# Kernel tuning notes

Hardware: AMD Instinct MI355X
Metric: run time of the kernel (lower is better)

Reference implementation:

```python
import jax, jax.numpy as jnp
import numpy as np

EPS = 1e-12  # torch F.normalize eps

def _l2norm(t, axis):
    n = jnp.linalg.norm(t, axis=axis, keepdims=True)
    return t / jnp.maximum(n, EPS)

def setup_inputs() -> dict:
    key = jax.random.key(0)
    ks = jax.random.split(key, 7)
    B, L, D, F, K = 16, 128, 512, 1024, 16
    return {
        "x": jax.random.normal(ks[0], (B, L, D), jnp.float32),
        "W_gate_basis": jax.random.normal(ks[1], (K, D, F), jnp.float32) * (1.0 / np.sqrt(D)),
        "W_up_basis": jax.random.normal(ks[2], (K, D, F), jnp.float32) * (1.0 / np.sqrt(D)),
        "W_down_basis": jax.random.normal(ks[3], (K, F, D), jnp.float32) * (1.0 / np.sqrt(F)),
        "token_coef1": jax.random.normal(ks[4], (L, K), jnp.float32),
        "token_coef2": jax.random.normal(ks[5], (L, K), jnp.float32),
        "token_coef3": jax.random.normal(ks[6], (L, K), jnp.float32),
        "u_scale_param": jnp.ones((1, F), jnp.float32),
        "v_scale_param": jnp.ones((1, F), jnp.float32),
    }

def reference(x, W_gate_basis, W_up_basis, W_down_basis,
              token_coef1, token_coef2, token_coef3,
              u_scale_param, v_scale_param):
    D = x.shape[-1]
    c1 = jax.nn.softmax(token_coef1, axis=-1)
    c2 = jax.nn.softmax(token_coef2, axis=-1)
    c3 = jax.nn.softmax(token_coef3, axis=-1)
    # per-token weights [L, D, F] / [L, F, D]
    W_gate = jnp.einsum('lk,kio->lio', c1, W_gate_basis)
    W_up = jnp.einsum('lk,kio->lio', c2, W_up_basis)
    W_down = jnp.einsum('lk,koj->loj', c3, W_down_basis)
    W_gate = _l2norm(W_gate, axis=1)   # normalize over input dim D
    W_up = _l2norm(W_up, axis=1)
    W_down = _l2norm(W_down, axis=1)   # normalize over hidden dim F
    u = jnp.einsum('bld,ldf->blf', x, W_gate)
    v = jnp.einsum('bld,ldf->blf', x, W_up)
    u_scale = jnp.abs(u_scale_param) * 1.0
    v_scale = jnp.abs(v_scale_param) * jnp.sqrt(jnp.float32(D))
    h = jax.nn.silu(v_scale * v) * (u_scale * u)
    out = jnp.einsum('blf,lfd->bld', h, W_down)
    return _l2norm(out, axis=-1)
```

## Files before the change

kernel.cpp:

```cpp
#include <hip/hip_runtime.h>
#include <hip/hip_bf16.h>
#include <cmath>


typedef _Float16 half8 __attribute__((ext_vector_type(8)));
typedef _Float16 half4 __attribute__((ext_vector_type(4)));
typedef float    f32x4 __attribute__((ext_vector_type(4)));

#define MFMA_F16 __builtin_amdgcn_mfma_f32_16x16x32_f16

static constexpr size_t OFF_P1 = 0;
static constexpr size_t OFF_P2 = 16777216;
static constexpr size_t OFF_P3 = 33554432;
static constexpr size_t OFF_HP = 50331648;
static constexpr size_t WS_FAST = OFF_HP + 4194304;

__global__ __launch_bounds__(256) void prep_basis_all(
    const float* __restrict__ wg, const float* __restrict__ wu,
    const float* __restrict__ wd,
    _Float16* __restrict__ P1, _Float16* __restrict__ P2,
    _Float16* __restrict__ P3, int zoff)
{
    int z = blockIdx.y + zoff;
    const float* src = (z == 0) ? wg : (z == 1) ? wu : wd;
    _Float16*    dst = (z == 0) ? P1 : (z == 1) ? P2 : P3;
    int Amin = (z == 2) ? 1024 : 512;
    int Bmaj = (z == 2) ? 512 : 1024;
    int nM = Bmaj >> 4;
    int m0 = (blockIdx.x / nM) * 32;
    int M0 = (blockIdx.x % nM) * 16;

    __shared__ float S[16 * 544];
    int t = threadIdx.x;

    int row = (t >> 2) & 31;
    int cg  = t & 3;
    int khi = t >> 7;
#pragma unroll
    for (int p = 0; p < 8; ++p) {
        int k = p * 2 + khi;
        f32x4 v = *(const f32x4*)(
            src + (size_t)k * Amin * Bmaj + (size_t)(m0 + row) * Bmaj + M0 + cg * 4);
#pragma unroll
        for (int j = 0; j < 4; ++j)
            S[k * 544 + row * 17 + cg * 4 + j] = v[j];
    }
    __syncthreads();

    int mn = t & 31, mjb = t >> 5;
#pragma unroll
    for (int q = 0; q < 2; ++q) {
        int mj = mjb + q * 8;
        half8 v0, v1;
#pragma unroll
        for (int k = 0; k < 8; ++k) v0[k] = (_Float16)S[k * 544 + mn * 17 + mj];
#pragma unroll
        for (int k = 0; k < 8; ++k) v1[k] = (_Float16)S[(k + 8) * 544 + mn * 17 + mj];
        _Float16* out = dst + ((size_t)(M0 + mj) * Amin + m0 + mn) * 16;
        *(half8*)out       = v0;
        *(half8*)(out + 8) = v1;
    }
}

__global__ __launch_bounds__(256) void prep_x(
    const float* __restrict__ x, _Float16* __restrict__ XA)
{
    int idx = blockIdx.x * 256 + threadIdx.x;
    int d4 = idx & 127;
    int l  = (idx >> 7) & 127;
    int b  = idx >> 14;
    f32x4 v = *(const f32x4*)(x + ((size_t)(b * 128 + l) * 512 + d4 * 4));
    half4 h = { (_Float16)v[0], (_Float16)v[1], (_Float16)v[2], (_Float16)v[3] };
    *(half4*)(XA + ((size_t)(l * 16 + b) * 512 + d4 * 4)) = h;
}

__global__ __launch_bounds__(256, 2) void up_fast(
    const _Float16* __restrict__ P1, const _Float16* __restrict__ P2,
    const _Float16* __restrict__ XA,
    const float* __restrict__ tc1, const float* __restrict__ tc2,
    const float* __restrict__ usp, const float* __restrict__ vsp,
    _Float16* __restrict__ Hp)
{
    int lg = blockIdx.x >> 6;
    int f0 = (blockIdx.x & 63) * 16;
    int tid = threadIdx.x;
    int w = tid >> 6, lane = tid & 63;
    int n = lane & 15, kc = lane >> 4;

    __shared__ __align__(16) _Float16 Wt[2][16 * 584];
    __shared__ float CN[2 * 256];

    if (tid < 32) {
        int s = tid >> 4, ll = tid & 15;
        const float* row = (s ? tc2 : tc1) + (size_t)(lg * 16 + ll) * 16;
        float e[16], m = -1e30f, sum = 0.f;
#pragma unroll
        for (int k = 0; k < 16; ++k) m = fmaxf(m, row[k]);
#pragma unroll
        for (int k = 0; k < 16; ++k) { e[k] = __expf(row[k] - m); sum += e[k]; }
        float r = 1.f / sum;
#pragma unroll
        for (int k = 0; k < 16; ++k) CN[s * 256 + ll * 16 + k] = e[k] * r;
    }
    __syncthreads();

    half8 cf1 = { 0, 0, 0, 0, 0, 0, 0, 0 };
    half8 cf2 = { 0, 0, 0, 0, 0, 0, 0, 0 };
    if (kc < 2) {
#pragma unroll
        for (int j = 0; j < 8; ++j) {
            cf1[j] = (_Float16)CN[0 * 256 + n * 16 + kc * 8 + j];
            cf2[j] = (_Float16)CN[1 * 256 + n * 16 + kc * 8 + j];
        }
    }

    f32x4 zf = { 0.f, 0.f, 0.f, 0.f };
    f32x4 aU[4], aV[4];
#pragma unroll
    for (int i = 0; i < 4; ++i) { aU[i] = zf; aV[i] = zf; }
    float nsqU[4] = { 0.f, 0.f, 0.f, 0.f };
    float nsqV[4] = { 0.f, 0.f, 0.f, 0.f };
    half8 xf[4];
    half8 pa[2][4][2];

    for (int it = 0; it < 16; ++it) {
        int d0 = it * 32;
#pragma unroll
        for (int m = 0; m < 2; ++m) {
            const _Float16* P = m ? P2 : P1;
#pragma unroll
            for (int fl = 0; fl < 4; ++fl)
#pragma unroll
                for (int dg = 0; dg < 2; ++dg) {
                    half8 a = { 0, 0, 0, 0, 0, 0, 0, 0 };
                    if (kc < 2)
                        a = *(const half8*)(P +
                            ((size_t)(f0 + w * 4 + fl) * 512 + d0 + dg * 16 + n) * 16 + kc * 8);
                    pa[m][fl][dg] = a;
                }
        }
        if (it > 0) {
#pragma unroll
            for (int li = 0; li < 4; ++li) {
                int l = w * 4 + li;
                half8 wU = *(const half8*)(&Wt[0][l * 584 + n * 36 + kc * 8]);
                half8 wV = *(const half8*)(&Wt[1][l * 584 + n * 36 + kc * 8]);
                aU[li] = MFMA_F16(xf[li], wU, aU[li], 0, 0, 0);
                aV[li] = MFMA_F16(xf[li], wV, aV[li], 0, 0, 0);
            }
        }
#pragma unroll
        for (int li = 0; li < 4; ++li) {
            int l = lg * 16 + w * 4 + li;
            xf[li] = *(const half8*)(XA + ((size_t)l * 16 + n) * 512 + d0 + kc * 8);
        }
        __syncthreads();
#pragma unroll
        for (int fl = 0; fl < 4; ++fl) {
            int f_l = w * 4 + fl;
#pragma unroll
            for (int dg = 0; dg < 2; ++dg) {
                f32x4 c1 = MFMA_F16(pa[0][fl][dg], cf1, zf, 0, 0, 0);
                nsqU[fl] += c1[0] * c1[0] + c1[1] * c1[1]
                          + c1[2] * c1[2] + c1[3] * c1[3];
                half4 h1 = { (_Float16)c1[0], (_Float16)c1[1],
                             (_Float16)c1[2], (_Float16)c1[3] };
                *(half4*)(&Wt[0][n * 584 + f_l * 36 + dg * 16 + kc * 4]) = h1;
                f32x4 c2 = MFMA_F16(pa[1][fl][dg], cf2, zf, 0, 0, 0);
                nsqV[fl] += c2[0] * c2[0] + c2[1] * c2[1]
                          + c2[2] * c2[2] + c2[3] * c2[3];
                half4 h2 = { (_Float16)c2[0], (_Float16)c2[1],
                             (_Float16)c2[2], (_Float16)c2[3] };
                *(half4*)(&Wt[1][n * 584 + f_l * 36 + dg * 16 + kc * 4]) = h2;
            }
        }
        __syncthreads();
    }
#pragma unroll
    for (int li = 0; li < 4; ++li) {
        int l = w * 4 + li;
        half8 wU = *(const half8*)(&Wt[0][l * 584 + n * 36 + kc * 8]);
        half8 wV = *(const half8*)(&Wt[1][l * 584 + n * 36 + kc * 8]);
        aU[li] = MFMA_F16(xf[li], wU, aU[li], 0, 0, 0);
        aV[li] = MFMA_F16(xf[li], wV, aV[li], 0, 0, 0);
    }

#pragma unroll
    for (int fl = 0; fl < 4; ++fl) {
        float vU = nsqU[fl], vV = nsqV[fl];
        vU += __shfl_xor(vU, 16); vU += __shfl_xor(vU, 32);
        vV += __shfl_xor(vV, 16); vV += __shfl_xor(vV, 32);
        if (kc == 0) {
            CN[0 * 256 + n * 16 + w * 4 + fl] = vU;
            CN[1 * 256 + n * 16 + w * 4 + fl] = vV;
        }
    }
    __syncthreads();

    int f = f0 + n;
    float usv = fabsf(usp[f]);
    float vsv = fabsf(vsp[f]) * 22.627416997969522f;
#pragma unroll
    for (int li = 0; li < 4; ++li) {
        int lgl = lg * 16 + w * 4 + li;
        float r1 = 1.f / fmaxf(sqrtf(CN[0 * 256 + (w * 4 + li) * 16 + n]), 1e-12f);
        float r2 = 1.f / fmaxf(sqrtf(CN[1 * 256 + (w * 4 + li) * 16 + n]), 1e-12f);
#pragma unroll
        for (int i = 0; i < 4; ++i) {
            float u = aU[li][i] * r1;
            float v = aV[li][i] * r2;
            float zz = vsv * v;
            float sil = zz / (1.f + __expf(-zz));
            float h = sil * (usv * u);
            Hp[((size_t)lgl * 16 + kc * 4 + i) * 1024 + f] = (_Float16)h;
        }
    }
}

__global__ __launch_bounds__(256, 2) void down_fast(
    const _Float16* __restrict__ P3, const float* __restrict__ tc3,
    const _Float16* __restrict__ Hp,
    float* __restrict__ Rp, float* __restrict__ Np)
{
    int zh = blockIdx.x >> 8;
    int rem = blockIdx.x & 255;
    int lg = rem >> 5;
    int d0 = (rem & 31) * 16;
    int tid = threadIdx.x;
    int w = tid >> 6, lane = tid & 63;
    int n = lane & 15, kc = lane >> 4;

    __shared__ __align__(16) _Float16 Wt[16 * 584];
    __shared__ float CN[256];

    if (tid < 16) {
        const float* row = tc3 + (size_t)(lg * 16 + tid) * 16;
        float e[16], m = -1e30f, sum = 0.f;
#pragma unroll
        for (int k = 0; k < 16; ++k) m = fmaxf(m, row[k]);
#pragma unroll
        for (int k = 0; k < 16; ++k) { e[k] = __expf(row[k] - m); sum += e[k]; }
        float r = 1.f / sum;
#pragma unroll
        for (int k = 0; k < 16; ++k) CN[tid * 16 + k] = e[k] * r;
    }
    __syncthreads();

    half8 cf3 = { 0, 0, 0, 0, 0, 0, 0, 0 };
    if (kc < 2) {
#pragma unroll
        for (int j = 0; j < 8; ++j)
            cf3[j] = (_Float16)CN[n * 16 + kc * 8 + j];
    }

    f32x4 zf = { 0.f, 0.f, 0.f, 0.f };
    f32x4 aO[4];
#pragma unroll
    for (int i = 0; i < 4; ++i) aO[i] = zf;
    float nsqD[4] = { 0.f, 0.f, 0.f, 0.f };
    half8 hf[4];
    half8 pa[4][2];

    for (int it = 0; it < 8; ++it) {
        int f0 = zh * 256 + it * 32;
#pragma unroll
        for (int dl = 0; dl < 4; ++dl) {
#pragma unroll
            for (int fg = 0; fg < 2; ++fg) {
                half8 a = { 0, 0, 0, 0, 0, 0, 0, 0 };
                if (kc < 2)
                    a = *(const half8*)(P3 +
                        ((size_t)(d0 + w * 4 + dl) * 1024 + f0 + fg * 16 + n) * 16 + kc * 8);
                pa[dl][fg] = a;
            }
        }
        if (it > 0) {
#pragma unroll
            for (int li = 0; li < 4; ++li) {
                int l = w * 4 + li;
                half8 wf = *(const half8*)(&Wt[l * 584 + n * 36 + kc * 8]);
                aO[li] = MFMA_F16(hf[li], wf, aO[li], 0, 0, 0);
            }
        }
#pragma unroll
        for (int li = 0; li < 4; ++li) {
            int l = lg * 16 + w * 4 + li;
            hf[li] = *(const half8*)(Hp + ((size_t)l * 16 + n) * 1024 + f0 + kc * 8);
        }
        __syncthreads();
#pragma unroll
        for (int dl = 0; dl < 4; ++dl) {
            int d_l = w * 4 + dl;
#pragma unroll
            for (int fg = 0; fg < 2; ++fg) {
                f32x4 cw = MFMA_F16(pa[dl][fg], cf3, zf, 0, 0, 0);
                nsqD[dl] += cw[0] * cw[0] + cw[1] * cw[1]
                          + cw[2] * cw[2] + cw[3] * cw[3];
                half4 h4 = { (_Float16)cw[0], (_Float16)cw[1],
                             (_Float16)cw[2], (_Float16)cw[3] };
                *(half4*)(&Wt[n * 584 + d_l * 36 + fg * 16 + kc * 4]) = h4;
            }
        }
        __syncthreads();
    }
#pragma unroll
    for (int li = 0; li < 4; ++li) {
        int l = w * 4 + li;
        half8 wf = *(const half8*)(&Wt[l * 584 + n * 36 + kc * 8]);
        aO[li] = MFMA_F16(hf[li], wf, aO[li], 0, 0, 0);
    }

#pragma unroll
    for (int dl = 0; dl < 4; ++dl) {
        float v = nsqD[dl];
        v += __shfl_xor(v, 16); v += __shfl_xor(v, 32);
        if (kc == 0)
            Np[(size_t)zh * 65536 + (size_t)(lg * 16 + n) * 512 + d0 + w * 4 + dl] = v;
    }
#pragma unroll
    for (int li = 0; li < 4; ++li) {
        int lgl = lg * 16 + w * 4 + li;
#pragma unroll
        for (int i = 0; i < 4; ++i)
            Rp[(size_t)zh * 1048576 +
               ((size_t)(kc * 4 + i) * 128 + lgl) * 512 + d0 + n] = aO[li][i];
    }
}

__global__ __launch_bounds__(128) void final_combine(
    const float* __restrict__ Rp, const float* __restrict__ Np,
    float* __restrict__ out)
{
    int rid = blockIdx.x;
    int l = rid & 127;
    int t = threadIdx.x;
    f32x4 r = { 0.f, 0.f, 0.f, 0.f };
    f32x4 nn = { 0.f, 0.f, 0.f, 0.f };
#pragma unroll
    for (int zh = 0; zh < 4; ++zh) {
        f32x4 rz = *(const f32x4*)(Rp + (size_t)zh * 1048576 + (size_t)rid * 512 + t * 4);
        f32x4 nz = *(const f32x4*)(Np + (size_t)zh * 65536 + (size_t)l * 512 + t * 4);
#pragma unroll
        for (int j = 0; j < 4; ++j) { r[j] += rz[j]; nn[j] += nz[j]; }
    }
    f32x4 y;
#pragma unroll
    for (int j = 0; j < 4; ++j) {
        float rr = 1.f / fmaxf(sqrtf(fmaxf(nn[j], 0.f)), 1e-12f);
        y[j] = r[j] * rr;
    }
    float s = y[0] * y[0] + y[1] * y[1] + y[2] * y[2] + y[3] * y[3];
#pragma unroll
    for (int off = 32; off > 0; off >>= 1) s += __shfl_down(s, off);
    __shared__ float sred[2];
    if ((t & 63) == 0) sred[t >> 6] = s;
    __syncthreads();
    float rr = 1.f / fmaxf(sqrtf(sred[0] + sred[1]), 1e-12f);
    f32x4 o = { y[0] * rr, y[1] * rr, y[2] * rr, y[3] * rr };
    *(f32x4*)(out + (size_t)rid * 512 + t * 4) = o;
}

__global__ __launch_bounds__(256) void up_kernel(
    const float* __restrict__ x,
    const float* __restrict__ wg, const float* __restrict__ wu,
    const float* __restrict__ tc1, const float* __restrict__ tc2,
    const float* __restrict__ usp, const float* __restrict__ vsp,
    _Float16* __restrict__ Hp)
{
    int lg = blockIdx.x >> 6;
    int f0 = (blockIdx.x & 63) * 16;
    int tid = threadIdx.x;
    int w = tid >> 6, lane = tid & 63;
    int n = lane & 15, kc = lane >> 4;

    __shared__ __align__(16) _Float16 Xt[256 * 40];
    __shared__ __align__(16) _Float16 Bh[32 * 16 * 24];
    __shared__ __align__(16) _Float16 Wt[16 * 528];
    __shared__ float CN[2 * 16 * 16];

    if (tid < 32) {
        int s = tid >> 4, ll = tid & 15;
        const float* row = (s ? tc2 : tc1) + (size_t)(lg * 16 + ll) * 16;
        float e[16], m = -1e30f, sum = 0.f;
#pragma unroll
        for (int k = 0; k < 16; ++k) m = fmaxf(m, row[k]);
#pragma unroll
        for (int k = 0; k < 16; ++k) { e[k] = __expf(row[k] - m); sum += e[k]; }
        float r = 1.f / sum;
#pragma unroll
        for (int k = 0; k < 16; ++k) CN[s * 256 + ll * 16 + k] = e[k] * r;
    }
    __syncthreads();

    half8 cf1 = { 0, 0, 0, 0, 0, 0, 0, 0 };
    half8 cf2 = { 0, 0, 0, 0, 0, 0, 0, 0 };
    if (kc < 2) {
#pragma unroll
        for (int j = 0; j < 8; ++j) {
            cf1[j] = (_Float16)CN[0 * 256 + n * 16 + kc * 8 + j];
            cf2[j] = (_Float16)CN[1 * 256 + n * 16 + kc * 8 + j];
        }
    }

    f32x4 zf = { 0.f, 0.f, 0.f, 0.f };
    f32x4 aU[4], aV[4];
#pragma unroll
    for (int i = 0; i < 4; ++i) { aU[i] = zf; aV[i] = zf; }
    float nsqU[4] = { 0.f, 0.f, 0.f, 0.f };
    float nsqV[4] = { 0.f, 0.f, 0.f, 0.f };

    for (int it = 0; it < 16; ++it) {
        int d0 = it * 32;
#pragma unroll
        for (int p = 0; p < 8; ++p) {
            int r = p * 32 + (tid >> 3);
            int fj = tid & 7;
            int ll = r >> 4, b = r & 15;
            f32x4 v = *(const f32x4*)(
                x + ((size_t)(b * 128 + lg * 16 + ll) * 512 + d0 + fj * 4));
            half4 h = { (_Float16)v[0], (_Float16)v[1],
                        (_Float16)v[2], (_Float16)v[3] };
            *(half4*)(&Xt[r * 40 + fj * 4]) = h;
        }
#pragma unroll
        for (int p = 0; p < 8; ++p) {
            int idx = p * 256 + tid;
            int q = idx & 3, dd = (idx >> 2) & 31, k = idx >> 7;
            f32x4 v = *(const f32x4*)(
                wg + ((size_t)k * 512 + d0 + dd) * 1024 + f0 + q * 4);
#pragma unroll
            for (int j = 0; j < 4; ++j)
                Bh[(dd * 16 + q * 4 + j) * 24 + k] = (_Float16)v[j];
        }
        __syncthreads();
#pragma unroll
        for (int fl = 0; fl < 4; ++fl) {
            int f_l = w * 4 + fl;
#pragma unroll
            for (int dg = 0; dg < 2; ++dg) {
                half8 a = { 0, 0, 0, 0, 0, 0, 0, 0 };
                if (kc < 2)
                    a = *(const half8*)(&Bh[((dg * 16 + n) * 16 + f_l) * 24 + kc * 8]);
                f32x4 cw = MFMA_F16(a, cf1, zf, 0, 0, 0);
                nsqU[fl] += cw[0] * cw[0] + cw[1] * cw[1]
                          + cw[2] * cw[2] + cw[3] * cw[3];
                half4 h4 = { (_Float16)cw[0], (_Float16)cw[1],
                             (_Float16)cw[2], (_Float16)cw[3] };
                *(half4*)(&Wt[n * 528 + f_l * 32 + dg * 16 + kc * 4]) = h4;
            }
        }
        __syncthreads();
#pragma unroll
        for (int li = 0; li < 4; ++li) {
            int l = w * 4 + li;
            half8 xf = *(const half8*)(&Xt[(l * 16 + n) * 40 + kc * 8]);
            half8 wf = *(const half8*)(&Wt[l * 528 + n * 32 + kc * 8]);
            aU[li] = MFMA_F16(xf, wf, aU[li], 0, 0, 0);
        }
#pragma unroll
        for (int p = 0; p < 8; ++p) {
            int idx = p * 256 + tid;
            int q = idx & 3, dd = (idx >> 2) & 31, k = idx >> 7;
            f32x4 v = *(const f32x4*)(
                wu + ((size_t)k * 512 + d0 + dd) * 1024 + f0 + q * 4);
#pragma unroll
            for (int j = 0; j < 4; ++j)
                Bh[(dd * 16 + q * 4 + j) * 24 + k] = (_Float16)v[j];
        }
        __syncthreads();
#pragma unroll
        for (int fl = 0; fl < 4; ++fl) {
            int f_l = w * 4 + fl;
#pragma unroll
            for (int dg = 0; dg < 2; ++dg) {
                half8 a = { 0, 0, 0, 0, 0, 0, 0, 0 };
                if (kc < 2)
                    a = *(const half8*)(&Bh[((dg * 16 + n) * 16 + f_l) * 24 + kc * 8]);
                f32x4 cw = MFMA_F16(a, cf2, zf, 0, 0, 0);
                nsqV[fl] += cw[0] * cw[0] + cw[1] * cw[1]
                          + cw[2] * cw[2] + cw[3] * cw[3];
                half4 h4 = { (_Float16)cw[0], (_Float16)cw[1],
                             (_Float16)cw[2], (_Float16)cw[3] };
                *(half4*)(&Wt[n * 528 + f_l * 32 + dg * 16 + kc * 4]) = h4;
            }
        }
        __syncthreads();
#pragma unroll
        for (int li = 0; li < 4; ++li) {
            int l = w * 4 + li;
            half8 xf = *(const half8*)(&Xt[(l * 16 + n) * 40 + kc * 8]);
            half8 wf = *(const half8*)(&Wt[l * 528 + n * 32 + kc * 8]);
            aV[li] = MFMA_F16(xf, wf, aV[li], 0, 0, 0);
        }
        __syncthreads();
    }

#pragma unroll
    for (int fl = 0; fl < 4; ++fl) {
        float vU = nsqU[fl], vV = nsqV[fl];
        vU += __shfl_xor(vU, 16); vU += __shfl_xor(vU, 32);
        vV += __shfl_xor(vV, 16); vV += __shfl_xor(vV, 32);
        if (kc == 0) {
            CN[0 * 256 + n * 16 + w * 4 + fl] = vU;
            CN[1 * 256 + n * 16 + w * 4 + fl] = vV;
        }
    }
    __syncthreads();

    int f = f0 + n;
    float usv = fabsf(usp[f]);
    float vsv = fabsf(vsp[f]) * 22.627416997969522f;
#pragma unroll
    for (int li = 0; li < 4; ++li) {
        int lgl = lg * 16 + w * 4 + li;
        float r1 = 1.f / fmaxf(sqrtf(CN[0 * 256 + (w * 4 + li) * 16 + n]), 1e-12f);
        float r2 = 1.f / fmaxf(sqrtf(CN[1 * 256 + (w * 4 + li) * 16 + n]), 1e-12f);
#pragma unroll
        for (int i = 0; i < 4; ++i) {
            float u = aU[li][i] * r1;
            float v = aV[li][i] * r2;
            float zz = vsv * v;
            float sil = zz / (1.f + __expf(-zz));
            float h = sil * (usv * u);
            Hp[((size_t)lgl * 16 + kc * 4 + i) * 1024 + f] = (_Float16)h;
        }
    }
}

__global__ __launch_bounds__(256) void down_kernel(
    const float* __restrict__ wd, const float* __restrict__ tc3,
    const _Float16* __restrict__ Hp, float* __restrict__ out)
{
    int lg = blockIdx.x >> 5;
    int d0 = (blockIdx.x & 31) * 16;
    int tid = threadIdx.x;
    int w = tid >> 6, lane = tid & 63;
    int n = lane & 15, kc = lane >> 4;

    __shared__ __align__(16) _Float16 Ht[256 * 40];
    __shared__ __align__(16) _Float16 Bh[32 * 16 * 24];
    __shared__ __align__(16) _Float16 Wt[16 * 528];
    __shared__ float CN[16 * 16];

    if (tid < 16) {
        const float* row = tc3 + (size_t)(lg * 16 + tid) * 16;
        float e[16], m = -1e30f, sum = 0.f;
#pragma unroll
        for (int k = 0; k < 16; ++k) m = fmaxf(m, row[k]);
#pragma unroll
        for (int k = 0; k < 16; ++k) { e[k] = __expf(row[k] - m); sum += e[k]; }
        float r = 1.f / sum;
#pragma unroll
        for (int k = 0; k < 16; ++k) CN[tid * 16 + k] = e[k] * r;
    }
    __syncthreads();

    half8 cf3 = { 0, 0, 0, 0, 0, 0, 0, 0 };
    if (kc < 2) {
#pragma unroll
        for (int j = 0; j < 8; ++j)
            cf3[j] = (_Float16)CN[n * 16 + kc * 8 + j];
    }

    f32x4 zf = { 0.f, 0.f, 0.f, 0.f };
    f32x4 aO[4];
#pragma unroll
    for (int i = 0; i < 4; ++i) aO[i] = zf;
    float nsqD[4] = { 0.f, 0.f, 0.f, 0.f };

    for (int it = 0; it < 32; ++it) {
        int f0 = it * 32;
#pragma unroll
        for (int p = 0; p < 8; ++p) {
            int r = p * 32 + (tid >> 3);
            int hj = tid & 7;
            int ll = r >> 4, b = r & 15;
            half4 v = *(const half4*)(
                Hp + ((size_t)(lg * 16 + ll) * 16 + b) * 1024 + f0 + hj * 4);
            *(half4*)(&Ht[r * 40 + hj * 4]) = v;
        }
#pragma unroll
        for (int p = 0; p < 8; ++p) {
            int idx = p * 256 + tid;
            int q = idx & 3, ff = (idx >> 2) & 31, k = idx >> 7;
            f32x4 v = *(const f32x4*)(
                wd + ((size_t)k * 1024 + f0 + ff) * 512 + d0 + q * 4);
#pragma unroll
            for (int j = 0; j < 4; ++j)
                Bh[(ff * 16 + q * 4 + j) * 24 + k] = (_Float16)v[j];
        }
        __syncthreads();
#pragma unroll
        for (int dl = 0; dl < 4; ++dl) {
            int d_l = w * 4 + dl;
#pragma unroll
            for (int fg = 0; fg < 2; ++fg) {
                half8 a = { 0, 0, 0, 0, 0, 0, 0, 0 };
                if (kc < 2)
                    a = *(const half8*)(&Bh[((fg * 16 + n) * 16 + d_l) * 24 + kc * 8]);
                f32x4 cw = MFMA_F16(a, cf3, zf, 0, 0, 0);
                nsqD[dl] += cw[0] * cw[0] + cw[1] * cw[1]
                          + cw[2] * cw[2] + cw[3] * cw[3];
                half4 h4 = { (_Float16)cw[0], (_Float16)cw[1],
                             (_Float16)cw[2], (_Float16)cw[3] };
                *(half4*)(&Wt[n * 528 + d_l * 32 + fg * 16 + kc * 4]) = h4;
            }
        }
        __syncthreads();
#pragma unroll
        for (int li = 0; li < 4; ++li) {
            int l = w * 4 + li;
            half8 hf = *(const half8*)(&Ht[(l * 16 + n) * 40 + kc * 8]);
            half8 wf = *(const half8*)(&Wt[l * 528 + n * 32 + kc * 8]);
            aO[li] = MFMA_F16(hf, wf, aO[li], 0, 0, 0);
        }
        __syncthreads();
    }

#pragma unroll
    for (int dl = 0; dl < 4; ++dl) {
        float v = nsqD[dl];
        v += __shfl_xor(v, 16); v += __shfl_xor(v, 32);
        if (kc == 0) CN[n * 16 + w * 4 + dl] = v;
    }
    __syncthreads();

#pragma unroll
    for (int li = 0; li < 4; ++li) {
        int lgl = lg * 16 + w * 4 + li;
        float r3 = 1.f / fmaxf(sqrtf(CN[(w * 4 + li) * 16 + n]), 1e-12f);
#pragma unroll
        for (int i = 0; i < 4; ++i)
            out[((size_t)(kc * 4 + i) * 128 + lgl) * 512 + d0 + n] = aO[li][i] * r3;
    }
}

__global__ __launch_bounds__(128) void final_kernel(float* __restrict__ out)
{
    int rid = blockIdx.x;
    int t = threadIdx.x;
    f32x4 y = *(const f32x4*)(out + (size_t)rid * 512 + t * 4);
    float s = y[0] * y[0] + y[1] * y[1] + y[2] * y[2] + y[3] * y[3];
#pragma unroll
    for (int off = 32; off > 0; off >>= 1) s += __shfl_down(s, off);
    __shared__ float sred[2];
    if ((t & 63) == 0) sred[t >> 6] = s;
    __syncthreads();
    float rr = 1.f / fmaxf(sqrtf(sred[0] + sred[1]), 1e-12f);
    f32x4 o = { y[0] * rr, y[1] * rr, y[2] * rr, y[3] * rr };
    *(f32x4*)(out + (size_t)rid * 512 + t * 4) = o;
}

extern "C" void kernel_launch(void* const* d_in, const int* in_sizes, int n_in,
                              void* d_out, int out_size, void* d_ws, size_t ws_size,
                              hipStream_t stream)
{
    (void)in_sizes; (void)n_in; (void)out_size;
    const float* x   = (const float*)d_in[0];
    const float* wg  = (const float*)d_in[1];
    const float* wu  = (const float*)d_in[2];
    const float* wd  = (const float*)d_in[3];
    const float* tc1 = (const float*)d_in[4];
    const float* tc2 = (const float*)d_in[5];
    const float* tc3 = (const float*)d_in[6];
    const float* usp = (const float*)d_in[7];
    const float* vsp = (const float*)d_in[8];
    float* outp = (float*)d_out;
    char* ws = (char*)d_ws;

    if (ws_size >= WS_FAST) {
        _Float16* P1 = (_Float16*)(ws + OFF_P1);
        _Float16* P2 = (_Float16*)(ws + OFF_P2);
        _Float16* P3 = (_Float16*)(ws + OFF_P3);
        _Float16* XA = (_Float16*)(ws + OFF_P3);
        _Float16* Hp = (_Float16*)(ws + OFF_HP);
        float* Rp = (float*)(ws + OFF_P1);
        float* Np = (float*)(ws + OFF_P2);
        prep_basis_all<<<dim3(1024, 2), dim3(256), 0, stream>>>(
            wg, wu, wd, P1, P2, P3, 0);
        prep_x<<<dim3(1024), dim3(256), 0, stream>>>(x, XA);
        up_fast<<<dim3(512), dim3(256), 0, stream>>>(P1, P2, XA, tc1, tc2,
                                                     usp, vsp, Hp);
        prep_basis_all<<<dim3(1024, 1), dim3(256), 0, stream>>>(
            wg, wu, wd, P1, P2, P3, 2);
        down_fast<<<dim3(1024), dim3(256), 0, stream>>>(P3, tc3, Hp, Rp, Np);
        final_combine<<<dim3(2048), dim3(128), 0, stream>>>(Rp, Np, outp);
    } else {
        _Float16* Hp = (_Float16*)ws;
        up_kernel<<<dim3(512), dim3(256), 0, stream>>>(x, wg, wu, tc1, tc2,
                                                       usp, vsp, Hp);
        down_kernel<<<dim3(256), dim3(256), 0, stream>>>(wd, tc3, Hp, outp);
        final_kernel<<<dim3(2048), dim3(128), 0, stream>>>(outp);
    }
}
```

Baseline: 233.9 us.

## Split up_fast reduction dimension across two wavegroups with LDS combine

Doubles the up_fast block to 512 threads. Two groups of four waves each handle half of the D reduction, and group 1's partial accumulators and norm sums go through shared memory to group 0, which applies the normalization and SiLU epilogue. The aim is more waves per CU to hide load and MFMA latency in the 16-iteration serial loop. In exchange, LDS use per block doubles and an extra cross-group reduction with barriers is added, which may limit occupancy.

```diff
diff --git a/kernel.cpp b/kernel.cpp
--- a/kernel.cpp
+++ b/kernel.cpp
@@ -74,7 +74,7 @@
     *(half4*)(XA + ((size_t)(l * 16 + b) * 512 + d4 * 4)) = h;
 }
 
-__global__ __launch_bounds__(256, 2) void up_fast(
+__global__ __launch_bounds__(512, 4) void up_fast(
     const _Float16* __restrict__ P1, const _Float16* __restrict__ P2,
     const _Float16* __restrict__ XA,
     const float* __restrict__ tc1, const float* __restrict__ tc2,
@@ -84,11 +84,13 @@
     int lg = blockIdx.x >> 6;
     int f0 = (blockIdx.x & 63) * 16;
     int tid = threadIdx.x;
-    int w = tid >> 6, lane = tid & 63;
+    int g = tid >> 8;
+    int w = (tid >> 6) & 3;
+    int lane = tid & 63;
     int n = lane & 15, kc = lane >> 4;
 
-    __shared__ __align__(16) _Float16 Wt[2][16 * 584];
-    __shared__ float CN[2 * 256];
+    __shared__ __align__(16) _Float16 Wt[2][2][16 * 584];
+    __shared__ float CN[4 * 256];
 
     if (tid < 32) {
         int s = tid >> 4, ll = tid & 15;
@@ -123,8 +125,8 @@
     half8 xf[4];
     half8 pa[2][4][2];
 
-    for (int it = 0; it < 16; ++it) {
-        int d0 = it * 32;
+    for (int it = 0; it < 8; ++it) {
+        int d0 = (g << 8) + it * 32;
 #pragma unroll
         for (int m = 0; m < 2; ++m) {
             const _Float16* P = m ? P2 : P1;
@@ -143,8 +145,8 @@
 #pragma unroll
             for (int li = 0; li < 4; ++li) {
                 int l = w * 4 + li;
-                half8 wU = *(const half8*)(&Wt[0][l * 584 + n * 36 + kc * 8]);
-                half8 wV = *(const half8*)(&Wt[1][l * 584 + n * 36 + kc * 8]);
+                half8 wU = *(const half8*)(&Wt[g][0][l * 584 + n * 36 + kc * 8]);
+                half8 wV = *(const half8*)(&Wt[g][1][l * 584 + n * 36 + kc * 8]);
                 aU[li] = MFMA_F16(xf[li], wU, aU[li], 0, 0, 0);
                 aV[li] = MFMA_F16(xf[li], wV, aV[li], 0, 0, 0);
             }
@@ -165,13 +167,13 @@
                           + c1[2] * c1[2] + c1[3] * c1[3];
                 half4 h1 = { (_Float16)c1[0], (_Float16)c1[1],
                              (_Float16)c1[2], (_Float16)c1[3] };
-                *(half4*)(&Wt[0][n * 584 + f_l * 36 + dg * 16 + kc * 4]) = h1;
+                *(half4*)(&Wt[g][0][n * 584 + f_l * 36 + dg * 16 + kc * 4]) = h1;
                 f32x4 c2 = MFMA_F16(pa[1][fl][dg], cf2, zf, 0, 0, 0);
                 nsqV[fl] += c2[0] * c2[0] + c2[1] * c2[1]
                           + c2[2] * c2[2] + c2[3] * c2[3];
                 half4 h2 = { (_Float16)c2[0], (_Float16)c2[1],
                              (_Float16)c2[2], (_Float16)c2[3] };
-                *(half4*)(&Wt[1][n * 584 + f_l * 36 + dg * 16 + kc * 4]) = h2;
+                *(half4*)(&Wt[g][1][n * 584 + f_l * 36 + dg * 16 + kc * 4]) = h2;
             }
         }
         __syncthreads();
@@ -179,8 +181,8 @@
 #pragma unroll
     for (int li = 0; li < 4; ++li) {
         int l = w * 4 + li;
-        half8 wU = *(const half8*)(&Wt[0][l * 584 + n * 36 + kc * 8]);
-        half8 wV = *(const half8*)(&Wt[1][l * 584 + n * 36 + kc * 8]);
+        half8 wU = *(const half8*)(&Wt[g][0][l * 584 + n * 36 + kc * 8]);
+        half8 wV = *(const half8*)(&Wt[g][1][l * 584 + n * 36 + kc * 8]);
         aU[li] = MFMA_F16(xf[li], wU, aU[li], 0, 0, 0);
         aV[li] = MFMA_F16(xf[li], wV, aV[li], 0, 0, 0);
     }
@@ -191,28 +193,48 @@
         vU += __shfl_xor(vU, 16); vU += __shfl_xor(vU, 32);
         vV += __shfl_xor(vV, 16); vV += __shfl_xor(vV, 32);
         if (kc == 0) {
-            CN[0 * 256 + n * 16 + w * 4 + fl] = vU;
-            CN[1 * 256 + n * 16 + w * 4 + fl] = vV;
-        }
-    }
-    __syncthreads();
-
-    int f = f0 + n;
-    float usv = fabsf(usp[f]);
-    float vsv = fabsf(vsp[f]) * 22.627416997969522f;
-#pragma unroll
-    for (int li = 0; li < 4; ++li) {
-        int lgl = lg * 16 + w * 4 + li;
-        float r1 = 1.f / fmaxf(sqrtf(CN[0 * 256 + (w * 4 + li) * 16 + n]), 1e-12f);
-        float r2 = 1.f / fmaxf(sqrtf(CN[1 * 256 + (w * 4 + li) * 16 + n]), 1e-12f);
-#pragma unroll
-        for (int i = 0; i < 4; ++i) {
-            float u = aU[li][i] * r1;
-            float v = aV[li][i] * r2;
-            float zz = vsv * v;
-            float sil = zz / (1.f + __expf(-zz));
-            float h = sil * (usv * u);
-            Hp[((size_t)lgl * 16 + kc * 4 + i) * 1024 + f] = (_Float16)h;
+            CN[(g << 9) + 0 * 256 + n * 16 + w * 4 + fl] = vU;
+            CN[(g << 9) + 1 * 256 + n * 16 + w * 4 + fl] = vV;
+        }
+    }
+    __syncthreads();
+
+    float* XB = (float*)(&Wt[1][0][0]);
+    if (g == 1) {
+#pragma unroll
+        for (int li = 0; li < 4; ++li)
+#pragma unroll
+            for (int i = 0; i < 4; ++i) {
+                int idx = ((w * 4 + li) * 16 + kc * 4 + i) * 16 + n;
+                XB[idx]        = aU[li][i];
+                XB[4096 + idx] = aV[li][i];
+            }
+    }
+    __syncthreads();
+
+    if (g == 0) {
+        int f = f0 + n;
+        float usv = fabsf(usp[f]);
+        float vsv = fabsf(vsp[f]) * 22.627416997969522f;
+#pragma unroll
+        for (int li = 0; li < 4; ++li) {
+            int lgl = lg * 16 + w * 4 + li;
+            float s1 = CN[0 * 256 + (w * 4 + li) * 16 + n]
+                     + CN[512 + 0 * 256 + (w * 4 + li) * 16 + n];
+            float s2 = CN[1 * 256 + (w * 4 + li) * 16 + n]
+                     + CN[512 + 1 * 256 + (w * 4 + li) * 16 + n];
+            float r1 = 1.f / fmaxf(sqrtf(s1), 1e-12f);
+            float r2 = 1.f / fmaxf(sqrtf(s2), 1e-12f);
+#pragma unroll
+            for (int i = 0; i < 4; ++i) {
+                int idx = ((w * 4 + li) * 16 + kc * 4 + i) * 16 + n;
+                float u = (aU[li][i] + XB[idx]) * r1;
+                float v = (aV[li][i] + XB[4096 + idx]) * r2;
+                float zz = vsv * v;
+                float sil = zz / (1.f + __expf(-zz));
+                float h = sil * (usv * u);
+                Hp[((size_t)lgl * 16 + kc * 4 + i) * 1024 + f] = (_Float16)h;
+            }
         }
     }
 }
@@ -679,7 +701,7 @@
         prep_basis_all<<<dim3(1024, 2), dim3(256), 0, stream>>>(
             wg, wu, wd, P1, P2, P3, 0);
         prep_x<<<dim3(1024), dim3(256), 0, stream>>>(x, XA);
-        up_fast<<<dim3(512), dim3(256), 0, stream>>>(P1, P2, XA, tc1, tc2,
+        up_fast<<<dim3(512), dim3(512), 0, stream>>>(P1, P2, XA, tc1, tc2,
                                                      usp, vsp, Hp);
         prep_basis_all<<<dim3(1024, 1), dim3(256), 0, stream>>>(
             wg, wu, wd, P1, P2, P3, 2);
```

Result: slower. 366.0 us (+56.4%).

## Double-buffer LDS weight tiles and prefetch basis; retile X and H for coalesced MFMA loads

Applied to the files above, without the earlier changes.

Double-buffers the shared-memory mixed-weight tiles in up_fast and down_fast, so each iteration writes the next tile while reading the previous one. The basis prefetch for the next step is interleaved between the MFMA phases, which lets one barrier per iteration do the work of two. The X and H intermediates are repacked into an 8-element-chunk interleaved layout, so MFMA operand loads become contiguous 16-byte reads. prep_x now transposes through LDS with fewer blocks. The cost is twice the LDS footprint, which may limit occupancy, and higher register pressure from the prefetched fragments.

```diff
diff --git a/kernel.cpp b/kernel.cpp
--- a/kernel.cpp
+++ b/kernel.cpp
@@ -65,13 +65,28 @@
 __global__ __launch_bounds__(256) void prep_x(
     const float* __restrict__ x, _Float16* __restrict__ XA)
 {
-    int idx = blockIdx.x * 256 + threadIdx.x;
-    int d4 = idx & 127;
-    int l  = (idx >> 7) & 127;
-    int b  = idx >> 14;
-    f32x4 v = *(const f32x4*)(x + ((size_t)(b * 128 + l) * 512 + d4 * 4));
-    half4 h = { (_Float16)v[0], (_Float16)v[1], (_Float16)v[2], (_Float16)v[3] };
-    *(half4*)(XA + ((size_t)(l * 16 + b) * 512 + d4 * 4)) = h;
+    int l = blockIdx.x >> 1, bh = blockIdx.x & 1;
+    __shared__ __align__(16) _Float16 XT[8][524];
+    int t = threadIdx.x;
+
+    int bl = t >> 5, q = t & 31;
+    int b = bh * 8 + bl;
+#pragma unroll
+    for (int j = 0; j < 4; ++j) {
+        f32x4 v = *(const f32x4*)(x + ((size_t)(b * 128 + l) * 512 + j * 128 + q * 4));
+#pragma unroll
+        for (int i = 0; i < 4; ++i)
+            XT[bl][j * 128 + q * 4 + i] = (_Float16)v[i];
+    }
+    __syncthreads();
+
+    int c = t >> 2, bi = t & 3;
+#pragma unroll
+    for (int s = 0; s < 2; ++s) {
+        int blw = bi * 2 + s;
+        half8 h = *(const half8*)(&XT[blw][c * 8]);
+        *(half8*)(XA + (((size_t)(l * 64 + c) * 16 + bh * 8 + blw) * 8)) = h;
+    }
 }
 
 __global__ __launch_bounds__(256, 2) void up_fast(
@@ -87,8 +102,24 @@
     int w = tid >> 6, lane = tid & 63;
     int n = lane & 15, kc = lane >> 4;
 
-    __shared__ __align__(16) _Float16 Wt[2][16 * 584];
+    __shared__ __align__(16) _Float16 Wt[2][2][16 * 584];
     __shared__ float CN[2 * 256];
+
+    half8 pa0[4][2], pa1[4][2];
+#pragma unroll
+    for (int fl = 0; fl < 4; ++fl)
+#pragma unroll
+        for (int dg = 0; dg < 2; ++dg) {
+            half8 a = { 0, 0, 0, 0, 0, 0, 0, 0 };
+            half8 b = { 0, 0, 0, 0, 0, 0, 0, 0 };
+            if (kc < 2) {
+                size_t off = ((size_t)(f0 + w * 4 + fl) * 512 + dg * 16 + n) * 16 + kc * 8;
+                a = *(const half8*)(P1 + off);
+                b = *(const half8*)(P2 + off);
+            }
+            pa0[fl][dg] = a;
+            pa1[fl][dg] = b;
+        }
 
     if (tid < 32) {
         int s = tid >> 4, ll = tid & 15;
@@ -121,66 +152,87 @@
     float nsqU[4] = { 0.f, 0.f, 0.f, 0.f };
     float nsqV[4] = { 0.f, 0.f, 0.f, 0.f };
     half8 xf[4];
-    half8 pa[2][4][2];
 
     for (int it = 0; it < 16; ++it) {
         int d0 = it * 32;
-#pragma unroll
-        for (int m = 0; m < 2; ++m) {
-            const _Float16* P = m ? P2 : P1;
-#pragma unroll
-            for (int fl = 0; fl < 4; ++fl)
-#pragma unroll
-                for (int dg = 0; dg < 2; ++dg) {
-                    half8 a = { 0, 0, 0, 0, 0, 0, 0, 0 };
-                    if (kc < 2)
-                        a = *(const half8*)(P +
-                            ((size_t)(f0 + w * 4 + fl) * 512 + d0 + dg * 16 + n) * 16 + kc * 8);
-                    pa[m][fl][dg] = a;
-                }
-        }
-        if (it > 0) {
-#pragma unroll
-            for (int li = 0; li < 4; ++li) {
-                int l = w * 4 + li;
-                half8 wU = *(const half8*)(&Wt[0][l * 584 + n * 36 + kc * 8]);
-                half8 wV = *(const half8*)(&Wt[1][l * 584 + n * 36 + kc * 8]);
-                aU[li] = MFMA_F16(xf[li], wU, aU[li], 0, 0, 0);
-                aV[li] = MFMA_F16(xf[li], wV, aV[li], 0, 0, 0);
-            }
-        }
-#pragma unroll
-        for (int li = 0; li < 4; ++li) {
-            int l = lg * 16 + w * 4 + li;
-            xf[li] = *(const half8*)(XA + ((size_t)l * 16 + n) * 512 + d0 + kc * 8);
-        }
-        __syncthreads();
+        _Float16* WtA = &Wt[it & 1][0][0];
+        _Float16* WtB = &Wt[it & 1][1][0];
+        const _Float16* RdA = &Wt[(it & 1) ^ 1][0][0];
+        const _Float16* RdB = &Wt[(it & 1) ^ 1][1][0];
+
 #pragma unroll
         for (int fl = 0; fl < 4; ++fl) {
             int f_l = w * 4 + fl;
 #pragma unroll
             for (int dg = 0; dg < 2; ++dg) {
-                f32x4 c1 = MFMA_F16(pa[0][fl][dg], cf1, zf, 0, 0, 0);
+                f32x4 c1 = MFMA_F16(pa0[fl][dg], cf1, zf, 0, 0, 0);
                 nsqU[fl] += c1[0] * c1[0] + c1[1] * c1[1]
                           + c1[2] * c1[2] + c1[3] * c1[3];
                 half4 h1 = { (_Float16)c1[0], (_Float16)c1[1],
                              (_Float16)c1[2], (_Float16)c1[3] };
-                *(half4*)(&Wt[0][n * 584 + f_l * 36 + dg * 16 + kc * 4]) = h1;
-                f32x4 c2 = MFMA_F16(pa[1][fl][dg], cf2, zf, 0, 0, 0);
+                *(half4*)(&WtA[n * 584 + f_l * 36 + dg * 16 + kc * 4]) = h1;
+            }
+        }
+        if (it < 15) {
+#pragma unroll
+            for (int fl = 0; fl < 4; ++fl)
+#pragma unroll
+                for (int dg = 0; dg < 2; ++dg) {
+                    half8 a = { 0, 0, 0, 0, 0, 0, 0, 0 };
+                    if (kc < 2)
+                        a = *(const half8*)(P1 +
+                            ((size_t)(f0 + w * 4 + fl) * 512 + d0 + 32 + dg * 16 + n) * 16 + kc * 8);
+                    pa0[fl][dg] = a;
+                }
+        }
+#pragma unroll
+        for (int fl = 0; fl < 4; ++fl) {
+            int f_l = w * 4 + fl;
+#pragma unroll
+            for (int dg = 0; dg < 2; ++dg) {
+                f32x4 c2 = MFMA_F16(pa1[fl][dg], cf2, zf, 0, 0, 0);
                 nsqV[fl] += c2[0] * c2[0] + c2[1] * c2[1]
                           + c2[2] * c2[2] + c2[3] * c2[3];
                 half4 h2 = { (_Float16)c2[0], (_Float16)c2[1],
                              (_Float16)c2[2], (_Float16)c2[3] };
-                *(half4*)(&Wt[1][n * 584 + f_l * 36 + dg * 16 + kc * 4]) = h2;
-            }
+                *(half4*)(&WtB[n * 584 + f_l * 36 + dg * 16 + kc * 4]) = h2;
+            }
+        }
+        if (it < 15) {
+#pragma unroll
+            for (int fl = 0; fl < 4; ++fl)
+#pragma unroll
+                for (int dg = 0; dg < 2; ++dg) {
+                    half8 a = { 0, 0, 0, 0, 0, 0, 0, 0 };
+                    if (kc < 2)
+                        a = *(const half8*)(P2 +
+                            ((size_t)(f0 + w * 4 + fl) * 512 + d0 + 32 + dg * 16 + n) * 16 + kc * 8);
+                    pa1[fl][dg] = a;
+                }
+        }
+        if (it > 0) {
+#pragma unroll
+            for (int li = 0; li < 4; ++li) {
+                int l = w * 4 + li;
+                half8 wU = *(const half8*)(&RdA[l * 584 + n * 36 + kc * 8]);
+                half8 wV = *(const half8*)(&RdB[l * 584 + n * 36 + kc * 8]);
+                aU[li] = MFMA_F16(xf[li], wU, aU[li], 0, 0, 0);
+                aV[li] = MFMA_F16(xf[li], wV, aV[li], 0, 0, 0);
+            }
+        }
+#pragma unroll
+        for (int li = 0; li < 4; ++li) {
+            int l = lg * 16 + w * 4 + li;
+            xf[li] = *(const half8*)(XA +
+                (((size_t)l * 64 + (d0 >> 3) + kc) * 16 + n) * 8);
         }
         __syncthreads();
     }
 #pragma unroll
     for (int li = 0; li < 4; ++li) {
         int l = w * 4 + li;
-        half8 wU = *(const half8*)(&Wt[0][l * 584 + n * 36 + kc * 8]);
-        half8 wV = *(const half8*)(&Wt[1][l * 584 + n * 36 + kc * 8]);
+        half8 wU = *(const half8*)(&Wt[1][0][l * 584 + n * 36 + kc * 8]);
+        half8 wV = *(const half8*)(&Wt[1][1][l * 584 + n * 36 + kc * 8]);
         aU[li] = MFMA_F16(xf[li], wU, aU[li], 0, 0, 0);
         aV[li] = MFMA_F16(xf[li], wV, aV[li], 0, 0, 0);
     }
@@ -212,7 +264,8 @@
             float zz = vsv * v;
             float sil = zz / (1.f + __expf(-zz));
             float h = sil * (usv * u);
-            Hp[((size_t)lgl * 16 + kc * 4 + i) * 1024 + f] = (_Float16)h;
+            Hp[(((size_t)lgl * 128 + (f >> 3)) * 16 + kc * 4 + i) * 8 + (f & 7)] =
+                (_Float16)h;
         }
     }
 }
@@ -230,8 +283,20 @@
     int w = tid >> 6, lane = tid & 63;
     int n = lane & 15, kc = lane >> 4;
 
-    __shared__ __align__(16) _Float16 Wt[16 * 584];
+    __shared__ __align__(16) _Float16 Wt[2][16 * 584];
     __shared__ float CN[256];
+
+    half8 pa[4][2];
+#pragma unroll
+    for (int dl = 0; dl < 4; ++dl)
+#pragma unroll
+        for (int fg = 0; fg < 2; ++fg) {
+            half8 a = { 0, 0, 0, 0, 0, 0, 0, 0 };
+            if (kc < 2)
+                a = *(const half8*)(P3 +
+                    ((size_t)(d0 + w * 4 + dl) * 1024 + zh * 256 + fg * 16 + n) * 16 + kc * 8);
+            pa[dl][fg] = a;
+        }
 
     if (tid < 16) {
         const float* row = tc3 + (size_t)(lg * 16 + tid) * 16;
@@ -259,35 +324,12 @@
     for (int i = 0; i < 4; ++i) aO[i] = zf;
     float nsqD[4] = { 0.f, 0.f, 0.f, 0.f };
     half8 hf[4];
-    half8 pa[4][2];
 
     for (int it = 0; it < 8; ++it) {
-        int f0 = zh * 256 + it * 32;
-#pragma unroll
-        for (int dl = 0; dl < 4; ++dl) {
-#pragma unroll
-            for (int fg = 0; fg < 2; ++fg) {
-                half8 a = { 0, 0, 0, 0, 0, 0, 0, 0 };
-                if (kc < 2)
-                    a = *(const half8*)(P3 +
-                        ((size_t)(d0 + w * 4 + dl) * 1024 + f0 + fg * 16 + n) * 16 + kc * 8);
-                pa[dl][fg] = a;
-            }
-        }
-        if (it > 0) {
-#pragma unroll
-            for (int li = 0; li < 4; ++li) {
-                int l = w * 4 + li;
-                half8 wf = *(const half8*)(&Wt[l * 584 + n * 36 + kc * 8]);
-                aO[li] = MFMA_F16(hf[li], wf, aO[li], 0, 0, 0);
-            }
-        }
-#pragma unroll
-        for (int li = 0; li < 4; ++li) {
-            int l = lg * 16 + w * 4 + li;
-            hf[li] = *(const half8*)(Hp + ((size_t)l * 16 + n) * 1024 + f0 + kc * 8);
-        }
-        __syncthreads();
+        int f0t = zh * 256 + it * 32;
+        _Float16* WtW = &Wt[it & 1][0];
+        const _Float16* WtR = &Wt[(it & 1) ^ 1][0];
+
 #pragma unroll
         for (int dl = 0; dl < 4; ++dl) {
             int d_l = w * 4 + dl;
@@ -298,15 +340,41 @@
                           + cw[2] * cw[2] + cw[3] * cw[3];
                 half4 h4 = { (_Float16)cw[0], (_Float16)cw[1],
                              (_Float16)cw[2], (_Float16)cw[3] };
-                *(half4*)(&Wt[n * 584 + d_l * 36 + fg * 16 + kc * 4]) = h4;
-            }
+                *(half4*)(&WtW[n * 584 + d_l * 36 + fg * 16 + kc * 4]) = h4;
+            }
+        }
+        if (it < 7) {
+#pragma unroll
+            for (int dl = 0; dl < 4; ++dl)
+#pragma unroll
+                for (int fg = 0; fg < 2; ++fg) {
+                    half8 a = { 0, 0, 0, 0, 0, 0, 0, 0 };
+                    if (kc < 2)
+                        a = *(const half8*)(P3 +
+                            ((size_t)(d0 + w * 4 + dl) * 1024 + f0t + 32 + fg * 16 + n) * 16 + kc * 8);
+                    pa[dl][fg] = a;
+                }
+        }
+        if (it > 0) {
+#pragma unroll
+            for (int li = 0; li < 4; ++li) {
+                int l = w * 4 + li;
+                half8 wf = *(const half8*)(&WtR[l * 584 + n * 36 + kc * 8]);
+                aO[li] = MFMA_F16(hf[li], wf, aO[li], 0, 0, 0);
+            }
+        }
+#pragma unroll
+        for (int li = 0; li < 4; ++li) {
+            int l = lg * 16 + w * 4 + li;
+            hf[li] = *(const half8*)(Hp +
+                (((size_t)l * 128 + (f0t >> 3) + kc) * 16 + n) * 8);
         }
         __syncthreads();
     }
 #pragma unroll
     for (int li = 0; li < 4; ++li) {
         int l = w * 4 + li;
-        half8 wf = *(const half8*)(&Wt[l * 584 + n * 36 + kc * 8]);
+        half8 wf = *(const half8*)(&Wt[1][l * 584 + n * 36 + kc * 8]);
         aO[li] = MFMA_F16(hf[li], wf, aO[li], 0, 0, 0);
     }
 
@@ -678,7 +746,7 @@
         float* Np = (float*)(ws + OFF_P2);
         prep_basis_all<<<dim3(1024, 2), dim3(256), 0, stream>>>(
             wg, wu, wd, P1, P2, P3, 0);
-        prep_x<<<dim3(1024), dim3(256), 0, stream>>>(x, XA);
+        prep_x<<<dim3(256), dim3(256), 0, stream>>>(x, XA);
         up_fast<<<dim3(512), dim3(256), 0, stream>>>(P1, P2, XA, tc1, tc2,
                                                      usp, vsp, Hp);
         prep_basis_all<<<dim3(1024, 1), dim3(256), 0, stream>>>(
```

Measured after the change: 243.9 us. 1.04x slower.
